# Kernel tuning notes

Hardware: AMD Instinct MI355X
Metric: run time of the kernel (lower is better)

## Reference

```python
import jax, jax.numpy as jnp
import numpy as np

# dims
B, L, DIN = 32, 1024, 8
D, KK, S = 128, 16, 8
K = (L - KK) // S + 1  # 127 patch tokens
NB, F = 4, 24
Q = 256.0  # Q8.8 scale


def _ste(x, y):
    # straight-through: forward = y (quantized), backward = identity
    return x + jax.lax.stop_gradient(y - x)


def q88(x):
    q = jnp.clip(jnp.round(x * Q), -32768.0, 32767.0) / Q
    return _ste(x, q)


def sig_lut(x):
    xq = q88(x)
    return q88(jax.nn.sigmoid(xq))


def silu_lut(x):
    xq = q88(x)
    return q88(xq * jax.nn.sigmoid(xq))


def layernorm(x, g, b, eps=1e-5):
    m = jnp.mean(x, axis=-1, keepdims=True)
    v = jnp.mean((x - m) ** 2, axis=-1, keepdims=True)
    return (x - m) * jax.lax.rsqrt(v + eps) * g + b


def conv1x1_q88(x, w, b):
    # x: (B, Cin, L); w: (Cout, Cin); Q8.8 integer-emulated pointwise conv
    y = jnp.einsum('bcl,oc->bol', q88(x), q88(w)) + q88(b)[None, :, None]
    return q88(y)


def conv1d_q88(x, w, b, stride):
    # x: (B, Cin, L); w: (Cout, Cin, k)
    y = jax.lax.conv_general_dilated(q88(x), q88(w), (stride,), 'VALID',
                                     dimension_numbers=('NCH', 'OIH', 'NCH'))
    return q88(y + q88(b)[None, :, None])


def ssm_scan(x, w_dt, b_dt):
    # x: (B, K, D). dt_proj acts along the time axis (Linear K->K), per source.
    # lam_all[b,t,d] = sigmoid_LUT(sum_k x[b,k,d] * w_dt[t,k] + b_dt[t])
    lam = sig_lut(jnp.einsum('bkd,tk->btd', x, w_dt) + b_dt[None, :, None])
    xs = jnp.moveaxis(x, 1, 0)      # (K, B, D)
    lams = jnp.moveaxis(lam, 1, 0)  # (K, B, D)

    def step(s, tu):
        lam_t, u_t = tu
        s = lam_t * s + (1.0 - lam_t) * u_t
        return s, s

    s0 = jnp.zeros(x.shape[::2], dtype=x.dtype)  # (B, D)
    _, ys = jax.lax.scan(step, s0, (lams, xs))
    return jnp.moveaxis(ys, 0, 1)  # (B, K, D)


def setup_inputs() -> dict:
    key = jax.random.key(0)
    ks = jax.random.split(key, 20)
    n = lambda k, sh, s=0.05: (jax.random.normal(k, sh, dtype=jnp.float32) * s)
    return {
        'x': jax.random.normal(ks[0], (B, L, DIN), dtype=jnp.float32),
        'w_proj': n(ks[1], (D, DIN), 0.2), 'b_proj': n(ks[2], (D,), 0.02),
        'w_patch': n(ks[3], (D, D, KK), 0.05), 'b_patch': n(ks[4], (D,), 0.02),
        'pe': n(ks[5], (K, D), 0.5), 'pe_scale': jnp.float32(1.0),
        'ln_g': jnp.ones((NB, D), jnp.float32), 'ln_b': jnp.zeros((NB, D), jnp.float32),
        'w_in': n(ks[6], (NB, D, D), 0.08), 'w_gate': n(ks[7], (NB, D, D), 0.08),
        'w_out': n(ks[8], (NB, D, D), 0.08),
        'w_dt': n(ks[9], (NB, K, K), 0.08), 'b_dt': n(ks[10], (NB, K), 0.02),
        'lnf_g': jnp.ones((D,), jnp.float32), 'lnf_b': jnp.zeros((D,), jnp.float32),
        'w_flat': n(ks[11], (D * F, D, K), 0.02), 'b_flat': n(ks[12], (D * F,), 0.02),
        'w_head': n(ks[13], (2, D), 0.1), 'b_head': n(ks[14], (2,), 0.02),
    }


def reference(x, w_proj, b_proj, w_patch, b_patch, pe, pe_scale,
              ln_g, ln_b, w_in, w_gate, w_out, w_dt, b_dt,
              lnf_g, lnf_b, w_flat, b_flat, w_head, b_head):
    xc = jnp.transpose(x, (0, 2, 1))                # (B, DIN, L)
    xp = conv1x1_q88(xc, w_proj, b_proj)            # (B, D, L)
    xe = conv1d_q88(xp, w_patch, b_patch, S)        # (B, D, K)
    h = jnp.transpose(xe, (0, 2, 1)) + pe_scale * pe[None]  # (B, K, D)
    for i in range(NB):
        hn = layernorm(h, ln_g[i], ln_b[i])
        u = silu_lut(jnp.einsum('bkd,de->bke', hn, w_in[i]))
        y = ssm_scan(u, w_dt[i], b_dt[i])
        g = silu_lut(jnp.einsum('bkd,de->bke', hn, w_gate[i]))
        h = h + jnp.einsum('bkd,de->bke', y * g, w_out[i])
    h = layernorm(h, lnf_g, lnf_b)
    xp2 = jnp.transpose(h, (0, 2, 1))               # (B, D, K)
    # output_layer_flat: full-length Conv1d kernel==K -> one giant contraction
    y_feat = q88(jnp.einsum('bdk,odk->bo', q88(xp2), q88(w_flat)) + q88(b_flat))
    y_feat = y_feat.reshape(x.shape[0], D, F)       # (B, D, F)
    out = conv1x1_q88(y_feat, w_head, b_head)       # (B, 2, F)
    return out
```

## Files before the change

kernel.cpp:

```cpp
#include <hip/hip_runtime.h>
#include <cmath>

#define DEV __device__ __forceinline__

namespace {

constexpr int Kp    = 127;
constexpr int Mrows = 32 * Kp;
constexpr int Rred  = 128 * Kp;

DEV float q88(float x) {
  float r = rintf(x * 256.0f);
  r = fminf(fmaxf(r, -32768.0f), 32767.0f);
  return r * 0.00390625f;
}
DEV float sigmoid_(float x) { return 1.0f / (1.0f + expf(-x)); }

DEV void fma16(const float4 av, const float4 bv, float (&acc)[4][4]) {
  acc[0][0] = fmaf(av.x, bv.x, acc[0][0]); acc[0][1] = fmaf(av.x, bv.y, acc[0][1]);
  acc[0][2] = fmaf(av.x, bv.z, acc[0][2]); acc[0][3] = fmaf(av.x, bv.w, acc[0][3]);
  acc[1][0] = fmaf(av.y, bv.x, acc[1][0]); acc[1][1] = fmaf(av.y, bv.y, acc[1][1]);
  acc[1][2] = fmaf(av.y, bv.z, acc[1][2]); acc[1][3] = fmaf(av.y, bv.w, acc[1][3]);
  acc[2][0] = fmaf(av.z, bv.x, acc[2][0]); acc[2][1] = fmaf(av.z, bv.y, acc[2][1]);
  acc[2][2] = fmaf(av.z, bv.z, acc[2][2]); acc[2][3] = fmaf(av.z, bv.w, acc[2][3]);
  acc[3][0] = fmaf(av.w, bv.x, acc[3][0]); acc[3][1] = fmaf(av.w, bv.y, acc[3][1]);
  acc[3][2] = fmaf(av.w, bv.z, acc[3][2]); acc[3][3] = fmaf(av.w, bv.w, acc[3][3]);
}

__global__ __launch_bounds__(256) void k_quant(
    const float* __restrict__ wproj, const float* __restrict__ bproj,
    const float* __restrict__ wpatch, const float* __restrict__ bpatch,
    const float* __restrict__ whead, const float* __restrict__ bhead,
    const float* __restrict__ bflat,
    float* __restrict__ wq_proj, float* __restrict__ bq_proj, float* __restrict__ wpq,
    float* __restrict__ bq_patch, float* __restrict__ wq_head, float* __restrict__ bq_head,
    float* __restrict__ bq_flat) {
  int i = blockIdx.x * 256 + threadIdx.x;
  if (i < 262144) {
    int j = i >> 14;
    int c = (i >> 7) & 127;
    int d = i & 127;
    wpq[i] = q88(wpatch[(d * 128 + c) * 16 + j]);
  }
  int t = i - 262144;
  if (t >= 0) {
    if      (t < 1024) wq_proj[t]         = q88(wproj[t]);
    else if (t < 1152) bq_proj[t - 1024]  = q88(bproj[t - 1024]);
    else if (t < 1280) bq_patch[t - 1152] = q88(bpatch[t - 1152]);
    else if (t < 1536) wq_head[t - 1280]  = q88(whead[t - 1280]);
    else if (t < 1538) bq_head[t - 1536]  = q88(bhead[t - 1536]);
    else if (t < 4610) bq_flat[t - 1538]  = q88(bflat[t - 1538]);
  }
}

__global__ __launch_bounds__(256) void k_proj(const float* __restrict__ x, const float* __restrict__ wq,
                                              const float* __restrict__ bq, float* __restrict__ xpq) {
  int bl0 = blockIdx.x * 16;
  int tid = threadIdx.x;
  __shared__ float xs[128];
  if (tid < 128) xs[tid] = q88(x[(size_t)bl0 * 8 + tid]);
  __syncthreads();
  int o = tid & 127;
  int half = tid >> 7;
  float wv[8];
#pragma unroll
  for (int c = 0; c < 8; ++c) wv[c] = wq[o * 8 + c];
  float bb = bq[o];
#pragma unroll
  for (int il = 0; il < 8; ++il) {
    int l_loc = half * 8 + il;
    float acc = bb;
#pragma unroll
    for (int c = 0; c < 8; ++c) acc = fmaf(xs[l_loc * 8 + c], wv[c], acc);
    xpq[(size_t)(bl0 + l_loc) * 128 + o] = q88(acc);
  }
}

__global__ __launch_bounds__(256) void k_patch(const float* __restrict__ xpq, const float* __restrict__ wpq,
                                               float* __restrict__ partJ) {
  __shared__ __align__(16) float As[128][36];
  int mt = blockIdx.x, jg = blockIdx.y;
  int tid = threadIdx.x;
  int mr = tid & 31, c0 = (tid >> 5) * 16;
  int tn = tid & 31, tm8 = tid >> 5;
  int m0 = mt * 32;
  int g = m0 + mr;
  int bb = g / 127, kq = g % 127;
  float acc[4][4] = {};
  for (int jj = 0; jj < 4; ++jj) {
    int j = jg * 4 + jj;
    const float* src = xpq + ((size_t)bb * 1024 + kq * 8 + j) * 128 + c0;
    __syncthreads();
#pragma unroll
    for (int q = 0; q < 4; ++q) {
      float4 v = *reinterpret_cast<const float4*>(src + q * 4);
      As[c0 + q * 4 + 0][mr] = v.x;
      As[c0 + q * 4 + 1][mr] = v.y;
      As[c0 + q * 4 + 2][mr] = v.z;
      As[c0 + q * 4 + 3][mr] = v.w;
    }
    __syncthreads();
    const float* wp = wpq + (size_t)j * 16384 + tn * 4;
#pragma unroll 4
    for (int c = 0; c < 128; ++c) {
      float4 bv = *reinterpret_cast<const float4*>(wp + c * 128);
      float4 av = *reinterpret_cast<const float4*>(&As[c][tm8 * 4]);
      fma16(av, bv, acc);
    }
  }
  float* dst = partJ + ((size_t)jg * Mrows + m0) * 128 + tn * 4;
#pragma unroll
  for (int i = 0; i < 4; ++i) {
    float4 o4 = make_float4(acc[i][0], acc[i][1], acc[i][2], acc[i][3]);
    *reinterpret_cast<float4*>(dst + (size_t)(tm8 * 4 + i) * 128) = o4;
  }
}

__global__ __launch_bounds__(256) void k_combine(const float* __restrict__ partJ, const float* __restrict__ bqp,
                                                 const float* __restrict__ pe, const float* __restrict__ pesc,
                                                 float* __restrict__ h) {
  int i = blockIdx.x * 256 + threadIdx.x;
  int n = i & 127;
  int gq = i >> 7;
  int k = gq % 127;
  float s = partJ[i] + partJ[520192 + i] + partJ[2 * 520192 + i] + partJ[3 * 520192 + i] + bqp[n];
  h[i] = q88(s) + pesc[0] * pe[k * 128 + n];
}

__global__ __launch_bounds__(256) void k_ln_ug(const float* __restrict__ h, const float* __restrict__ lng,
                                               const float* __restrict__ lnb, const float* __restrict__ Win,
                                               const float* __restrict__ Wgate, float* __restrict__ u,
                                               float* __restrict__ gbuf) {
  __shared__ __align__(16) float As[128][36];
  __shared__ float2 lnpart[8][32];
  __shared__ float mean_s[32], inv_s[32];
  const float* W = blockIdx.y ? Wgate : Win;
  float* out = blockIdx.y ? gbuf : u;
  int tid = threadIdx.x;
  int mr = tid & 31, c0 = (tid >> 5) * 16;
  int m0 = blockIdx.x * 32;
  const float* src = h + (size_t)(m0 + mr) * 128 + c0;
  float s1 = 0.f, s2 = 0.f;
#pragma unroll
  for (int q = 0; q < 4; ++q) {
    float4 v = *reinterpret_cast<const float4*>(src + q * 4);
    As[c0 + q * 4 + 0][mr] = v.x;
    As[c0 + q * 4 + 1][mr] = v.y;
    As[c0 + q * 4 + 2][mr] = v.z;
    As[c0 + q * 4 + 3][mr] = v.w;
    s1 += v.x + v.y + v.z + v.w;
    s2 = fmaf(v.x, v.x, s2); s2 = fmaf(v.y, v.y, s2);
    s2 = fmaf(v.z, v.z, s2); s2 = fmaf(v.w, v.w, s2);
  }
  lnpart[tid >> 5][mr] = make_float2(s1, s2);
  __syncthreads();
  if (tid < 32) {
    float s = 0.f, ss = 0.f;
#pragma unroll
    for (int j = 0; j < 8; ++j) { float2 p = lnpart[j][tid]; s += p.x; ss += p.y; }
    float mn = s * (1.0f / 128.0f);
    float var = ss * (1.0f / 128.0f) - mn * mn;
    mean_s[tid] = mn;
    inv_s[tid] = rsqrtf(var + 1e-5f);
  }
  __syncthreads();
  float mnv = mean_s[mr], invv = inv_s[mr];
#pragma unroll
  for (int q = 0; q < 16; ++q) {
    int c = c0 + q;
    As[c][mr] = (As[c][mr] - mnv) * invv * lng[c] + lnb[c];
  }
  __syncthreads();
  int tn = tid & 31, tm8 = tid >> 5;
  float acc[4][4] = {};
  const float* wp = W + tn * 4;
#pragma unroll 4
  for (int c = 0; c < 128; ++c) {
    float4 bv = *reinterpret_cast<const float4*>(wp + c * 128);
    float4 av = *reinterpret_cast<const float4*>(&As[c][tm8 * 4]);
    fma16(av, bv, acc);
  }
  float* dst = out + (size_t)m0 * 128 + tn * 4;
#pragma unroll
  for (int i = 0; i < 4; ++i) {
    float4 o4;
    { float xq = q88(acc[i][0]); o4.x = q88(xq * sigmoid_(xq)); }
    { float xq = q88(acc[i][1]); o4.y = q88(xq * sigmoid_(xq)); }
    { float xq = q88(acc[i][2]); o4.z = q88(xq * sigmoid_(xq)); }
    { float xq = q88(acc[i][3]); o4.w = q88(xq * sigmoid_(xq)); }
    *reinterpret_cast<float4*>(dst + (size_t)(tm8 * 4 + i) * 128) = o4;
  }
}

__global__ __launch_bounds__(256) void k_lamg(const float* __restrict__ u, const float* __restrict__ wdt,
                                              const float* __restrict__ bdt, float* __restrict__ lam) {
  __shared__ __align__(16) float Wk[32][36];
  __shared__ __align__(16) float Us[32][132];
  int b = blockIdx.x, tt = blockIdx.y;
  int t0 = tt * 32;
  int tid = threadIdx.x;
  int dg = tid & 31, tg = tid >> 5;
  float acc[4][4] = {};
  const float* ub = u + (size_t)b * (127 * 128);
  for (int k0 = 0; k0 < 127; k0 += 32) {
    __syncthreads();
    {
      int k = tid & 31, tl = tid >> 5;
#pragma unroll
      for (int q = 0; q < 4; ++q) {
        int t = tl + 8 * q;
        int tg2 = t0 + t, kg = k0 + k;
        float v = (tg2 < 127 && kg < 127) ? wdt[tg2 * 127 + kg] : 0.f;
        Wk[k][t] = v;
      }
    }
    {
      int dq = tid & 7, k = tid >> 3;
      int kg = k0 + k;
      const float* srcp = ub + (size_t)kg * 128 + dq * 16;
#pragma unroll
      for (int q = 0; q < 4; ++q) {
        float4 v = make_float4(0.f, 0.f, 0.f, 0.f);
        if (kg < 127) v = *reinterpret_cast<const float4*>(srcp + q * 4);
        *reinterpret_cast<float4*>(&Us[k][dq * 16 + q * 4]) = v;
      }
    }
    __syncthreads();
#pragma unroll 4
    for (int k = 0; k < 32; ++k) {
      float4 tv = *reinterpret_cast<const float4*>(&Wk[k][tg * 4]);
      float4 dv = *reinterpret_cast<const float4*>(&Us[k][dg * 4]);
      fma16(tv, dv, acc);
    }
  }
#pragma unroll
  for (int ti = 0; ti < 4; ++ti) {
    int t = t0 + tg * 4 + ti;
    if (t < 127) {
      float bb = bdt[t];
      float4 o4;
      o4.x = q88(sigmoid_(q88(acc[ti][0] + bb)));
      o4.y = q88(sigmoid_(q88(acc[ti][1] + bb)));
      o4.z = q88(sigmoid_(q88(acc[ti][2] + bb)));
      o4.w = q88(sigmoid_(q88(acc[ti][3] + bb)));
      *reinterpret_cast<float4*>(lam + ((size_t)b * 127 + t) * 128 + dg * 4) = o4;
    }
  }
}

__global__ __launch_bounds__(128) void k_scan(const float* __restrict__ u, const float* __restrict__ gbuf,
                                              float* __restrict__ lamp) {
  int gt = blockIdx.x * 128 + threadIdx.x;
  int b = gt >> 5, d4 = (gt & 31) * 4;
  size_t base = (size_t)b * (127 * 128) + d4;
  float4 s = make_float4(0.f, 0.f, 0.f, 0.f);
  for (int t = 0; t < 127; ++t) {
    size_t idx = base + (size_t)t * 128;
    float4 lm = *reinterpret_cast<const float4*>(lamp + idx);
    float4 uu = *reinterpret_cast<const float4*>(u + idx);
    float4 gg = *reinterpret_cast<const float4*>(gbuf + idx);
    s.x = lm.x * s.x + (1.0f - lm.x) * uu.x;
    s.y = lm.y * s.y + (1.0f - lm.y) * uu.y;
    s.z = lm.z * s.z + (1.0f - lm.z) * uu.z;
    s.w = lm.w * s.w + (1.0f - lm.w) * uu.w;
    float4 p = make_float4(s.x * gg.x, s.y * gg.y, s.z * gg.z, s.w * gg.w);
    *reinterpret_cast<float4*>(lamp + idx) = p;
  }
}

__global__ __launch_bounds__(256) void k_outproj(const float* __restrict__ p, const float* __restrict__ W,
                                                 float* __restrict__ h) {
  __shared__ __align__(16) float As[128][36];
  int tid = threadIdx.x;
  int mr = tid & 31, c0 = (tid >> 5) * 16;
  int m0 = blockIdx.x * 32;
  const float* src = p + (size_t)(m0 + mr) * 128 + c0;
#pragma unroll
  for (int q = 0; q < 4; ++q) {
    float4 v = *reinterpret_cast<const float4*>(src + q * 4);
    As[c0 + q * 4 + 0][mr] = v.x;
    As[c0 + q * 4 + 1][mr] = v.y;
    As[c0 + q * 4 + 2][mr] = v.z;
    As[c0 + q * 4 + 3][mr] = v.w;
  }
  __syncthreads();
  int tn = tid & 31, tm8 = tid >> 5;
  float acc[4][4] = {};
  const float* wp = W + tn * 4;
#pragma unroll 4
  for (int c = 0; c < 128; ++c) {
    float4 bv = *reinterpret_cast<const float4*>(wp + c * 128);
    float4 av = *reinterpret_cast<const float4*>(&As[c][tm8 * 4]);
    fma16(av, bv, acc);
  }
  float* dst = h + (size_t)m0 * 128 + tn * 4;
#pragma unroll
  for (int i = 0; i < 4; ++i) {
    float4 hv = *reinterpret_cast<float4*>(dst + (size_t)(tm8 * 4 + i) * 128);
    hv.x += acc[i][0]; hv.y += acc[i][1]; hv.z += acc[i][2]; hv.w += acc[i][3];
    *reinterpret_cast<float4*>(dst + (size_t)(tm8 * 4 + i) * 128) = hv;
  }
}

__global__ __launch_bounds__(128) void k_lnf(const float* __restrict__ h, const float* __restrict__ gg,
                                             const float* __restrict__ bb, float* __restrict__ xp2q) {
  int row = blockIdx.x;
  int d = threadIdx.x;
  float v = h[(size_t)row * 128 + d];
  __shared__ float red[128];
  __shared__ float mn_s, inv_s;
  red[d] = v;
  __syncthreads();
  for (int off = 64; off > 0; off >>= 1) {
    if (d < off) red[d] += red[d + off];
    __syncthreads();
  }
  if (d == 0) mn_s = red[0] * (1.0f / 128.0f);
  __syncthreads();
  float dv = v - mn_s;
  red[d] = dv * dv;
  __syncthreads();
  for (int off = 64; off > 0; off >>= 1) {
    if (d < off) red[d] += red[d + off];
    __syncthreads();
  }
  if (d == 0) inv_s = rsqrtf(red[0] * (1.0f / 128.0f) + 1e-5f);
  __syncthreads();
  float hn = (v - mn_s) * inv_s * gg[d] + bb[d];
  int b = row / 127, k = row % 127;
  xp2q[((size_t)b * 128 + d) * 127 + k] = q88(hn);
}

__global__ __launch_bounds__(128) void k_flat(const float* __restrict__ Aq, const float* __restrict__ Wf,
                                              float* __restrict__ partF) {
  __shared__ float As[32][36];
  __shared__ float Ws[32][260];
  int ot = blockIdx.x, rs = blockIdx.y;
  int tid = threadIdx.x;
  int og = tid & 31, bsub = tid >> 5;
  int o0 = ot * 256;
  int r0 = rs * 256;
  float acc[8][8] = {};

  for (int ch = 0; ch < 256; ch += 32) {
    int rb = r0 + ch;
    __syncthreads();
    {
      int b = tid & 31, q0 = tid >> 5;
#pragma unroll
      for (int qq = 0; qq < 2; ++qq) {
        int q = q0 + qq * 4;
        int rr = rb + q * 4;
        float4 v = make_float4(0.f, 0.f, 0.f, 0.f);
        if (rr < Rred) v = *reinterpret_cast<const float4*>(Aq + (size_t)b * Rred + rr);
        As[q * 4 + 0][b] = v.x * 0.00390625f;
        As[q * 4 + 1][b] = v.y * 0.00390625f;
        As[q * 4 + 2][b] = v.z * 0.00390625f;
        As[q * 4 + 3][b] = v.w * 0.00390625f;
      }
    }
#pragma unroll
    for (int pp = 0; pp < 2; ++pp) {
      int o_s = tid + pp * 128;
      const float* wrow = Wf + (size_t)(o0 + o_s) * Rred;
#pragma unroll
      for (int q = 0; q < 8; ++q) {
        int rr = rb + q * 4;
        float4 v = make_float4(0.f, 0.f, 0.f, 0.f);
        if (rr < Rred) v = *reinterpret_cast<const float4*>(wrow + rr);
        Ws[q * 4 + 0][o_s] = rintf(v.x * 256.0f);
        Ws[q * 4 + 1][o_s] = rintf(v.y * 256.0f);
        Ws[q * 4 + 2][o_s] = rintf(v.z * 256.0f);
        Ws[q * 4 + 3][o_s] = rintf(v.w * 256.0f);
      }
    }
    __syncthreads();
#pragma unroll 4
    for (int rl = 0; rl < 32; ++rl) {
      float4 a0 = *reinterpret_cast<const float4*>(&As[rl][bsub * 8]);
      float4 a1 = *reinterpret_cast<const float4*>(&As[rl][bsub * 8 + 4]);
      float4 w0 = *reinterpret_cast<const float4*>(&Ws[rl][og * 4]);
      float4 w1 = *reinterpret_cast<const float4*>(&Ws[rl][og * 4 + 128]);
      float a[8] = {a0.x, a0.y, a0.z, a0.w, a1.x, a1.y, a1.z, a1.w};
      float w[8] = {w0.x, w0.y, w0.z, w0.w, w1.x, w1.y, w1.z, w1.w};
#pragma unroll
      for (int bi = 0; bi < 8; ++bi) {
#pragma unroll
        for (int oi = 0; oi < 8; ++oi)
          acc[bi][oi] = fmaf(a[bi], w[oi], acc[bi][oi]);
      }
    }
  }
#pragma unroll
  for (int bi = 0; bi < 8; ++bi) {
    int b = bsub * 8 + bi;
    float* dst = partF + ((size_t)rs * 32 + b) * 3072 + o0;
    *reinterpret_cast<float4*>(dst + og * 4) =
        make_float4(acc[bi][0], acc[bi][1], acc[bi][2], acc[bi][3]);
    *reinterpret_cast<float4*>(dst + 128 + og * 4) =
        make_float4(acc[bi][4], acc[bi][5], acc[bi][6], acc[bi][7]);
  }
}

__global__ __launch_bounds__(256) void k_head(const float* __restrict__ partF, const float* __restrict__ bqf,
                                              const float* __restrict__ wqh, const float* __restrict__ bqh,
                                              float* __restrict__ out) {
  int b = blockIdx.x;
  int tid = threadIdx.x;
  __shared__ float yf[3072];
#pragma unroll
  for (int i = 0; i < 12; ++i) {
    int o = tid + 256 * i;
    float s = bqf[o];
    for (int rsq = 0; rsq < 64; ++rsq) s += partF[((size_t)rsq * 32 + b) * 3072 + o];
    yf[o] = q88(s);
  }
  __syncthreads();
  if (tid < 48) {
    int oh = tid / 24, f = tid % 24;
    float acc = bqh[oh];
    for (int d = 0; d < 128; ++d) acc = fmaf(yf[d * 24 + f], wqh[oh * 128 + d], acc);
    out[(size_t)b * 48 + oh * 24 + f] = q88(acc);
  }
}

}

extern "C" void kernel_launch(void* const* d_in, const int* in_sizes, int n_in,
                              void* d_out, int out_size, void* d_ws, size_t ws_size,
                              hipStream_t stream) {
  const float* x      = (const float*)d_in[0];
  const float* wproj  = (const float*)d_in[1];
  const float* bproj  = (const float*)d_in[2];
  const float* wpatch = (const float*)d_in[3];
  const float* bpatch = (const float*)d_in[4];
  const float* pe     = (const float*)d_in[5];
  const float* pescal = (const float*)d_in[6];
  const float* lng    = (const float*)d_in[7];
  const float* lnb    = (const float*)d_in[8];
  const float* win    = (const float*)d_in[9];
  const float* wgate  = (const float*)d_in[10];
  const float* wout   = (const float*)d_in[11];
  const float* wdt    = (const float*)d_in[12];
  const float* bdt    = (const float*)d_in[13];
  const float* lnfg   = (const float*)d_in[14];
  const float* lnfb   = (const float*)d_in[15];
  const float* wflat  = (const float*)d_in[16];
  const float* bflat  = (const float*)d_in[17];
  const float* whead  = (const float*)d_in[18];
  const float* bhead  = (const float*)d_in[19];
  float* out = (float*)d_out;
  float* ws  = (float*)d_ws;

  constexpr size_t O_WQPROJ  = 0;
  constexpr size_t O_BQPROJ  = 1024;
  constexpr size_t O_WPQ     = 2048;
  constexpr size_t O_BQPATCH = 264192;
  constexpr size_t O_WQHEAD  = 264320;
  constexpr size_t O_BQHEAD  = 264576;
  constexpr size_t O_BQFLAT  = 264704;
  constexpr size_t O_XPQ     = 267776;
  constexpr size_t O_PARTJ   = 4462080;
  constexpr size_t O_H       = 6542848;
  constexpr size_t O_U       = 7063040;
  constexpr size_t O_G       = 7583232;
  constexpr size_t O_LAMP    = 8103424;
  constexpr size_t O_XP2Q    = 8623616;
  constexpr size_t O_PARTF   = O_XPQ;

  k_quant<<<(262144 + 4610 + 255) / 256, 256, 0, stream>>>(
      wproj, bproj, wpatch, bpatch, whead, bhead, bflat,
      ws + O_WQPROJ, ws + O_BQPROJ, ws + O_WPQ, ws + O_BQPATCH,
      ws + O_WQHEAD, ws + O_BQHEAD, ws + O_BQFLAT);

  k_proj<<<2048, 256, 0, stream>>>(x, ws + O_WQPROJ, ws + O_BQPROJ, ws + O_XPQ);

  {
    dim3 g(127, 4);
    k_patch<<<g, 256, 0, stream>>>(ws + O_XPQ, ws + O_WPQ, ws + O_PARTJ);
  }
  k_combine<<<2032, 256, 0, stream>>>(ws + O_PARTJ, ws + O_BQPATCH, pe, pescal, ws + O_H);

  for (int i = 0; i < 4; ++i) {
    dim3 g4(127, 2);
    k_ln_ug<<<g4, 256, 0, stream>>>(ws + O_H, lng + i * 128, lnb + i * 128,
                                    win + (size_t)i * 16384, wgate + (size_t)i * 16384,
                                    ws + O_U, ws + O_G);
    {
      dim3 gl(32, 4);
      k_lamg<<<gl, 256, 0, stream>>>(ws + O_U, wdt + (size_t)i * 16129, bdt + (size_t)i * 127,
                                     ws + O_LAMP);
    }
    k_scan<<<8, 128, 0, stream>>>(ws + O_U, ws + O_G, ws + O_LAMP);
    k_outproj<<<127, 256, 0, stream>>>(ws + O_LAMP, wout + (size_t)i * 16384, ws + O_H);
  }

  k_lnf<<<4064, 128, 0, stream>>>(ws + O_H, lnfg, lnfb, ws + O_XP2Q);

  {
    dim3 g(12, 64);
    k_flat<<<g, 128, 0, stream>>>(ws + O_XP2Q, wflat, ws + O_PARTF);
  }
  k_head<<<32, 256, 0, stream>>>(ws + O_PARTF, ws + O_BQFLAT, ws + O_WQHEAD, ws + O_BQHEAD, out);
}
```

Before: 497.2 us.

## Fuse u/gate GEMMs, widen scan parallelism, shuffle LN, prefetch flat contraction

The input and gate projections now run in one kernel that shares the normalized activation tile across both weight matrices, halving the LayerNorm work and the tile loads. The scan now uses one thread per channel across 32 blocks instead of 8 blocks of float4 lanes, and keeps eight steps of loads in flight ahead of the serial recurrence. The final LayerNorm replaces its shared-memory tree reductions with wavefront shuffles. The flat contraction uses 128-wide output tiles over twice as many blocks, with a register prefetch of the next chunk so global loads overlap compute. The risks are higher register pressure and a smaller per-thread FMA tile in k_flat, which lowers arithmetic intensity.

```diff
diff --git a/kernel.cpp b/kernel.cpp
--- a/kernel.cpp
+++ b/kernel.cpp
@@ -127,15 +127,13 @@
   h[i] = q88(s) + pesc[0] * pe[k * 128 + n];
 }
 
-__global__ __launch_bounds__(256) void k_ln_ug(const float* __restrict__ h, const float* __restrict__ lng,
-                                               const float* __restrict__ lnb, const float* __restrict__ Win,
-                                               const float* __restrict__ Wgate, float* __restrict__ u,
-                                               float* __restrict__ gbuf) {
+__global__ __launch_bounds__(256) void k_ln_ug2(const float* __restrict__ h, const float* __restrict__ lng,
+                                                const float* __restrict__ lnb, const float* __restrict__ Win,
+                                                const float* __restrict__ Wgate, float* __restrict__ u,
+                                                float* __restrict__ gbuf) {
   __shared__ __align__(16) float As[128][36];
   __shared__ float2 lnpart[8][32];
   __shared__ float mean_s[32], inv_s[32];
-  const float* W = blockIdx.y ? Wgate : Win;
-  float* out = blockIdx.y ? gbuf : u;
   int tid = threadIdx.x;
   int mr = tid & 31, c0 = (tid >> 5) * 16;
   int m0 = blockIdx.x * 32;
@@ -172,23 +170,33 @@
   }
   __syncthreads();
   int tn = tid & 31, tm8 = tid >> 5;
-  float acc[4][4] = {};
-  const float* wp = W + tn * 4;
-#pragma unroll 4
+  float accU[4][4] = {}, accG[4][4] = {};
+  const float* wpU = Win + tn * 4;
+  const float* wpG = Wgate + tn * 4;
+#pragma unroll 2
   for (int c = 0; c < 128; ++c) {
-    float4 bv = *reinterpret_cast<const float4*>(wp + c * 128);
     float4 av = *reinterpret_cast<const float4*>(&As[c][tm8 * 4]);
-    fma16(av, bv, acc);
-  }
-  float* dst = out + (size_t)m0 * 128 + tn * 4;
+    float4 bu = *reinterpret_cast<const float4*>(wpU + c * 128);
+    fma16(av, bu, accU);
+    float4 bg = *reinterpret_cast<const float4*>(wpG + c * 128);
+    fma16(av, bg, accG);
+  }
+  float* dstU = u + (size_t)m0 * 128 + tn * 4;
+  float* dstG = gbuf + (size_t)m0 * 128 + tn * 4;
 #pragma unroll
   for (int i = 0; i < 4; ++i) {
     float4 o4;
-    { float xq = q88(acc[i][0]); o4.x = q88(xq * sigmoid_(xq)); }
-    { float xq = q88(acc[i][1]); o4.y = q88(xq * sigmoid_(xq)); }
-    { float xq = q88(acc[i][2]); o4.z = q88(xq * sigmoid_(xq)); }
-    { float xq = q88(acc[i][3]); o4.w = q88(xq * sigmoid_(xq)); }
-    *reinterpret_cast<float4*>(dst + (size_t)(tm8 * 4 + i) * 128) = o4;
+    { float xq = q88(accU[i][0]); o4.x = q88(xq * sigmoid_(xq)); }
+    { float xq = q88(accU[i][1]); o4.y = q88(xq * sigmoid_(xq)); }
+    { float xq = q88(accU[i][2]); o4.z = q88(xq * sigmoid_(xq)); }
+    { float xq = q88(accU[i][3]); o4.w = q88(xq * sigmoid_(xq)); }
+    *reinterpret_cast<float4*>(dstU + (size_t)(tm8 * 4 + i) * 128) = o4;
+    float4 g4;
+    { float xq = q88(accG[i][0]); g4.x = q88(xq * sigmoid_(xq)); }
+    { float xq = q88(accG[i][1]); g4.y = q88(xq * sigmoid_(xq)); }
+    { float xq = q88(accG[i][2]); g4.z = q88(xq * sigmoid_(xq)); }
+    { float xq = q88(accG[i][3]); g4.w = q88(xq * sigmoid_(xq)); }
+    *reinterpret_cast<float4*>(dstG + (size_t)(tm8 * 4 + i) * 128) = g4;
   }
 }
 
@@ -250,21 +258,35 @@
 
 __global__ __launch_bounds__(128) void k_scan(const float* __restrict__ u, const float* __restrict__ gbuf,
                                               float* __restrict__ lamp) {
-  int gt = blockIdx.x * 128 + threadIdx.x;
-  int b = gt >> 5, d4 = (gt & 31) * 4;
-  size_t base = (size_t)b * (127 * 128) + d4;
-  float4 s = make_float4(0.f, 0.f, 0.f, 0.f);
-  for (int t = 0; t < 127; ++t) {
-    size_t idx = base + (size_t)t * 128;
-    float4 lm = *reinterpret_cast<const float4*>(lamp + idx);
-    float4 uu = *reinterpret_cast<const float4*>(u + idx);
-    float4 gg = *reinterpret_cast<const float4*>(gbuf + idx);
-    s.x = lm.x * s.x + (1.0f - lm.x) * uu.x;
-    s.y = lm.y * s.y + (1.0f - lm.y) * uu.y;
-    s.z = lm.z * s.z + (1.0f - lm.z) * uu.z;
-    s.w = lm.w * s.w + (1.0f - lm.w) * uu.w;
-    float4 p = make_float4(s.x * gg.x, s.y * gg.y, s.z * gg.z, s.w * gg.w);
-    *reinterpret_cast<float4*>(lamp + idx) = p;
+  int b = blockIdx.x, d = threadIdx.x;
+  const size_t base = (size_t)b * (127 * 128) + d;
+  float lm[8], uu[8], gg[8];
+#pragma unroll
+  for (int j = 0; j < 8; ++j) {
+    size_t idx = base + (size_t)j * 128;
+    lm[j] = lamp[idx]; uu[j] = u[idx]; gg[j] = gbuf[idx];
+  }
+  float s = 0.f;
+  int t = 0;
+  for (int it = 0; it < 15; ++it) {
+#pragma unroll
+    for (int j = 0; j < 8; ++j) {
+      float l0 = lm[j], u0 = uu[j], g0 = gg[j];
+      s = l0 * s + (1.0f - l0) * u0;
+      lamp[base + (size_t)(t + j) * 128] = s * g0;
+      int tn = t + j + 8;
+      if (tn < 127) {
+        size_t idx = base + (size_t)tn * 128;
+        lm[j] = lamp[idx]; uu[j] = u[idx]; gg[j] = gbuf[idx];
+      }
+    }
+    t += 8;
+  }
+#pragma unroll
+  for (int j = 0; j < 7; ++j) {
+    float l0 = lm[j], u0 = uu[j], g0 = gg[j];
+    s = l0 * s + (1.0f - l0) * u0;
+    lamp[base + (size_t)(120 + j) * 128] = s * g0;
   }
 }
 
@@ -307,26 +329,20 @@
   int row = blockIdx.x;
   int d = threadIdx.x;
   float v = h[(size_t)row * 128 + d];
-  __shared__ float red[128];
-  __shared__ float mn_s, inv_s;
-  red[d] = v;
-  __syncthreads();
-  for (int off = 64; off > 0; off >>= 1) {
-    if (d < off) red[d] += red[d + off];
-    __syncthreads();
-  }
-  if (d == 0) mn_s = red[0] * (1.0f / 128.0f);
-  __syncthreads();
-  float dv = v - mn_s;
-  red[d] = dv * dv;
-  __syncthreads();
-  for (int off = 64; off > 0; off >>= 1) {
-    if (d < off) red[d] += red[d + off];
-    __syncthreads();
-  }
-  if (d == 0) inv_s = rsqrtf(red[0] * (1.0f / 128.0f) + 1e-5f);
-  __syncthreads();
-  float hn = (v - mn_s) * inv_s * gg[d] + bb[d];
+  float a = v, sq = v * v;
+#pragma unroll
+  for (int off = 32; off >= 1; off >>= 1) {
+    a += __shfl_xor(a, off, 64);
+    sq += __shfl_xor(sq, off, 64);
+  }
+  __shared__ float ps[2][2];
+  int w = d >> 6;
+  if ((d & 63) == 0) { ps[w][0] = a; ps[w][1] = sq; }
+  __syncthreads();
+  float S1 = ps[0][0] + ps[1][0], S2 = ps[0][1] + ps[1][1];
+  float mn = S1 * (1.0f / 128.0f);
+  float inv = rsqrtf(S2 * (1.0f / 128.0f) - mn * mn + 1e-5f);
+  float hn = (v - mn) * inv * gg[d] + bb[d];
   int b = row / 127, k = row % 127;
   xp2q[((size_t)b * 128 + d) * 127 + k] = q88(hn);
 }
@@ -334,71 +350,86 @@
 __global__ __launch_bounds__(128) void k_flat(const float* __restrict__ Aq, const float* __restrict__ Wf,
                                               float* __restrict__ partF) {
   __shared__ float As[32][36];
-  __shared__ float Ws[32][260];
+  __shared__ float Ws[32][132];
   int ot = blockIdx.x, rs = blockIdx.y;
   int tid = threadIdx.x;
   int og = tid & 31, bsub = tid >> 5;
-  int o0 = ot * 256;
+  int o0 = ot * 128;
   int r0 = rs * 256;
-  float acc[8][8] = {};
-
-  for (int ch = 0; ch < 256; ch += 32) {
-    int rb = r0 + ch;
+  float acc[8][4] = {};
+
+  const int wq4 = tid & 3;
+  const int wrow_l = tid >> 2;
+  const int aq = tid >> 5;
+  const int ab = tid & 31;
+
+  float4 wreg[4][2];
+  float4 areg[2];
+
+  auto loadch = [&](int rb) {
+#pragma unroll
+    for (int p = 0; p < 4; ++p) {
+      const float* wrow = Wf + (size_t)(o0 + wrow_l + 32 * p) * Rred;
+#pragma unroll
+      for (int q = 0; q < 2; ++q) {
+        int rr = rb + wq4 * 8 + q * 4;
+        wreg[p][q] = (rr < Rred) ? *reinterpret_cast<const float4*>(wrow + rr)
+                                 : make_float4(0.f, 0.f, 0.f, 0.f);
+      }
+    }
+#pragma unroll
+    for (int i = 0; i < 2; ++i) {
+      int rr = rb + aq * 4 + 16 * i;
+      areg[i] = (rr < Rred) ? *reinterpret_cast<const float4*>(Aq + (size_t)ab * Rred + rr)
+                            : make_float4(0.f, 0.f, 0.f, 0.f);
+    }
+  };
+
+  loadch(r0);
+  for (int ch = 0; ch < 8; ++ch) {
     __syncthreads();
-    {
-      int b = tid & 31, q0 = tid >> 5;
-#pragma unroll
-      for (int qq = 0; qq < 2; ++qq) {
-        int q = q0 + qq * 4;
-        int rr = rb + q * 4;
-        float4 v = make_float4(0.f, 0.f, 0.f, 0.f);
-        if (rr < Rred) v = *reinterpret_cast<const float4*>(Aq + (size_t)b * Rred + rr);
-        As[q * 4 + 0][b] = v.x * 0.00390625f;
-        As[q * 4 + 1][b] = v.y * 0.00390625f;
-        As[q * 4 + 2][b] = v.z * 0.00390625f;
-        As[q * 4 + 3][b] = v.w * 0.00390625f;
+#pragma unroll
+    for (int p = 0; p < 4; ++p) {
+      int oc = wrow_l + 32 * p;
+#pragma unroll
+      for (int q = 0; q < 2; ++q) {
+        int rl = wq4 * 8 + q * 4;
+        Ws[rl + 0][oc] = rintf(wreg[p][q].x * 256.0f);
+        Ws[rl + 1][oc] = rintf(wreg[p][q].y * 256.0f);
+        Ws[rl + 2][oc] = rintf(wreg[p][q].z * 256.0f);
+        Ws[rl + 3][oc] = rintf(wreg[p][q].w * 256.0f);
       }
     }
 #pragma unroll
-    for (int pp = 0; pp < 2; ++pp) {
-      int o_s = tid + pp * 128;
-      const float* wrow = Wf + (size_t)(o0 + o_s) * Rred;
-#pragma unroll
-      for (int q = 0; q < 8; ++q) {
-        int rr = rb + q * 4;
-        float4 v = make_float4(0.f, 0.f, 0.f, 0.f);
-        if (rr < Rred) v = *reinterpret_cast<const float4*>(wrow + rr);
-        Ws[q * 4 + 0][o_s] = rintf(v.x * 256.0f);
-        Ws[q * 4 + 1][o_s] = rintf(v.y * 256.0f);
-        Ws[q * 4 + 2][o_s] = rintf(v.z * 256.0f);
-        Ws[q * 4 + 3][o_s] = rintf(v.w * 256.0f);
-      }
+    for (int i = 0; i < 2; ++i) {
+      int rl = aq * 4 + 16 * i;
+      As[rl + 0][ab] = areg[i].x * 0.00390625f;
+      As[rl + 1][ab] = areg[i].y * 0.00390625f;
+      As[rl + 2][ab] = areg[i].z * 0.00390625f;
+      As[rl + 3][ab] = areg[i].w * 0.00390625f;
     }
     __syncthreads();
+    if (ch < 7) loadch(r0 + (ch + 1) * 32);
 #pragma unroll 4
     for (int rl = 0; rl < 32; ++rl) {
+      float4 w  = *reinterpret_cast<const float4*>(&Ws[rl][og * 4]);
       float4 a0 = *reinterpret_cast<const float4*>(&As[rl][bsub * 8]);
       float4 a1 = *reinterpret_cast<const float4*>(&As[rl][bsub * 8 + 4]);
-      float4 w0 = *reinterpret_cast<const float4*>(&Ws[rl][og * 4]);
-      float4 w1 = *reinterpret_cast<const float4*>(&Ws[rl][og * 4 + 128]);
       float a[8] = {a0.x, a0.y, a0.z, a0.w, a1.x, a1.y, a1.z, a1.w};
-      float w[8] = {w0.x, w0.y, w0.z, w0.w, w1.x, w1.y, w1.z, w1.w};
 #pragma unroll
       for (int bi = 0; bi < 8; ++bi) {
-#pragma unroll
-        for (int oi = 0; oi < 8; ++oi)
-          acc[bi][oi] = fmaf(a[bi], w[oi], acc[bi][oi]);
+        acc[bi][0] = fmaf(a[bi], w.x, acc[bi][0]);
+        acc[bi][1] = fmaf(a[bi], w.y, acc[bi][1]);
+        acc[bi][2] = fmaf(a[bi], w.z, acc[bi][2]);
+        acc[bi][3] = fmaf(a[bi], w.w, acc[bi][3]);
       }
     }
   }
 #pragma unroll
   for (int bi = 0; bi < 8; ++bi) {
     int b = bsub * 8 + bi;
-    float* dst = partF + ((size_t)rs * 32 + b) * 3072 + o0;
-    *reinterpret_cast<float4*>(dst + og * 4) =
-        make_float4(acc[bi][0], acc[bi][1], acc[bi][2], acc[bi][3]);
-    *reinterpret_cast<float4*>(dst + 128 + og * 4) =
-        make_float4(acc[bi][4], acc[bi][5], acc[bi][6], acc[bi][7]);
+    float* dst = partF + ((size_t)rs * 32 + b) * 3072 + o0 + og * 4;
+    *reinterpret_cast<float4*>(dst) = make_float4(acc[bi][0], acc[bi][1], acc[bi][2], acc[bi][3]);
   }
 }
 
@@ -482,23 +513,22 @@
   k_combine<<<2032, 256, 0, stream>>>(ws + O_PARTJ, ws + O_BQPATCH, pe, pescal, ws + O_H);
 
   for (int i = 0; i < 4; ++i) {
-    dim3 g4(127, 2);
-    k_ln_ug<<<g4, 256, 0, stream>>>(ws + O_H, lng + i * 128, lnb + i * 128,
-                                    win + (size_t)i * 16384, wgate + (size_t)i * 16384,
-                                    ws + O_U, ws + O_G);
+    k_ln_ug2<<<127, 256, 0, stream>>>(ws + O_H, lng + i * 128, lnb + i * 128,
+                                      win + (size_t)i * 16384, wgate + (size_t)i * 16384,
+                                      ws + O_U, ws + O_G);
     {
       dim3 gl(32, 4);
       k_lamg<<<gl, 256, 0, stream>>>(ws + O_U, wdt + (size_t)i * 16129, bdt + (size_t)i * 127,
                                      ws + O_LAMP);
     }
-    k_scan<<<8, 128, 0, stream>>>(ws + O_U, ws + O_G, ws + O_LAMP);
+    k_scan<<<32, 128, 0, stream>>>(ws + O_U, ws + O_G, ws + O_LAMP);
     k_outproj<<<127, 256, 0, stream>>>(ws + O_LAMP, wout + (size_t)i * 16384, ws + O_H);
   }
 
   k_lnf<<<4064, 128, 0, stream>>>(ws + O_H, lnfg, lnfb, ws + O_XP2Q);
 
   {
-    dim3 g(12, 64);
+    dim3 g(24, 64);
     k_flat<<<g, 128, 0, stream>>>(ws + O_XP2Q, wflat, ws + O_PARTF);
   }
   k_head<<<32, 256, 0, stream>>>(ws + O_PARTF, ws + O_BQFLAT, ws + O_WQHEAD, ws + O_BQHEAD, out);
```

After: 445.3 us. 10.4% less time.
